# Optimization experiments

Hardware: AMD Instinct MI355X
Metric: run time of the kernel (lower is better)

Reference implementation:

```python
import jax, jax.numpy as jnp
import numpy as np

NUM_HEADS = 12
NUM_LANDMARKS = 64
PINV_ITERS = 6


def moore_penrose_iter_pinv(x, iters=PINV_ITERS):
    # x: [..., m, m]
    abs_x = jnp.abs(x)
    col = abs_x.sum(axis=-1)
    row = abs_x.sum(axis=-2)
    z = jnp.swapaxes(x, -1, -2) / (jnp.max(col) * jnp.max(row))
    I = jnp.eye(x.shape[-1], dtype=x.dtype)
    for _ in range(iters):
        xz = x @ z
        z = 0.25 * z @ (13.0 * I - xz @ (15.0 * I - xz @ (7.0 * I - xz)))
    return z


def setup_inputs() -> dict:
    key = jax.random.key(0)
    k1, k2, k3, k4 = jax.random.split(key, 4)
    B, N, C = 2, 2048, 768
    x = jax.random.normal(k1, (B, N, C), dtype=jnp.float32)
    w_qkv = jax.random.normal(k2, (3 * C, C), dtype=jnp.float32) * 0.02
    w_proj = jax.random.normal(k3, (C, C), dtype=jnp.float32) * 0.02
    b_proj = jax.random.normal(k4, (C,), dtype=jnp.float32) * 0.02
    return {"x": x, "w_qkv": w_qkv, "w_proj": w_proj, "b_proj": b_proj}


def reference(x, w_qkv, w_proj, b_proj):
    B, N, C = x.shape
    H = NUM_HEADS
    m = NUM_LANDMARKS
    d = C // H
    scale = d ** -0.5
    original_N = N

    rem = N % m
    if rem > 0:  # pad at the FRONT of the sequence, as in the torch code
        x = jnp.pad(x, ((0, 0), (m - rem, 0), (0, 0)))
        N = x.shape[1]

    qkv = x @ w_qkv.T  # [B, N, 3C]
    q, k, v = jnp.split(qkv, 3, axis=-1)
    # [B, N, C] -> [B, H, N, d]
    to_heads = lambda t: t.reshape(B, N, H, d).transpose(0, 2, 1, 3)
    q, k, v = to_heads(q), to_heads(k), to_heads(v)
    q = q * scale

    l = N // m  # segment length per landmark (N is a multiple of m after padding)
    # '(n l) d -> n d' mean over l: landmarks [B, H, m, d]
    q_landmarks = q.reshape(B, H, m, l, d).mean(axis=3)
    k_landmarks = k.reshape(B, H, m, l, d).mean(axis=3)

    sim1 = jnp.einsum('bhnd,bhmd->bhnm', q, k_landmarks)          # [B,H,N,m]
    sim2 = jnp.einsum('bhid,bhjd->bhij', q_landmarks, k_landmarks)  # [B,H,m,m]
    sim3 = jnp.einsum('bhmd,bhnd->bhmn', q_landmarks, k)          # [B,H,m,N]

    attn1 = jax.nn.softmax(sim1, axis=-1)
    attn2 = jax.nn.softmax(sim2, axis=-1)
    attn3 = jax.nn.softmax(sim3, axis=-1)

    attn2_inv = moore_penrose_iter_pinv(attn2, PINV_ITERS)

    attn = (attn1 @ attn2_inv) @ attn3            # [B,H,N,N] full attention map
    out = attn1 @ (attn2_inv @ (attn3 @ v))       # [B,H,N,d]

    out = out.transpose(0, 2, 1, 3).reshape(B, N, C)
    out = out[:, -original_N:]
    out = out @ w_proj.T + b_proj
    return out, attn
```

## Files before the change

kernel.cpp:

```cpp
#include <hip/hip_runtime.h>
#include <math.h>

#define BQ 2
#define NQ 2048
#define CQ 768
#define HQ 12
#define DQ 64
#define MQ 64
#define LQ 32
#define C3 2304
#define BH 24
#define BN 4096

typedef short bf16x8 __attribute__((ext_vector_type(8)));
typedef float f32x4 __attribute__((ext_vector_type(4)));

__device__ inline void atomicMaxPosF(float* addr, float v) {
  atomicMax((int*)addr, __float_as_int(v));
}

__device__ inline void f2pair(float f, ushort& hi, ushort& lo) {
  union { float f; unsigned u; } a; a.f = f;
  hi = (ushort)(a.u >> 16);
  union { unsigned u; float f; } h; h.u = ((unsigned)hi) << 16;
  union { float f; unsigned u; } b; b.f = f - h.f;
  lo = (ushort)(b.u >> 16);
}

__device__ inline void stage_plane(const ushort* __restrict__ g, int ld,
                                   ushort* l, int t) {
#pragma unroll
  for (int i = 0; i < 4; ++i) {
    int flat = t + i * 256;
    int row = flat >> 3;
    int ch = (flat & 7) ^ (row & 7);
    __builtin_amdgcn_global_load_lds(
        (const __attribute__((address_space(1))) void*)(g + (size_t)row * ld + ch * 8),
        (__attribute__((address_space(3))) void*)(l + flat * 8), 16, 0, 0);
  }
}

__device__ inline bf16x8 rdfrag(const ushort* p, int row, int kb) {
  return *(const bf16x8*)((const char*)p + row * 128 + (kb ^ ((row & 7) << 4)));
}

__global__ __launch_bounds__(256) void gemm_bt3(
    const ushort* __restrict__ Ah, const ushort* __restrict__ Al,
    const ushort* __restrict__ Bh, const ushort* __restrict__ Bl,
    const float* __restrict__ bias, float* __restrict__ C,
    int Kdim, int lda, int ldb, int ldc, int qscale, int zH,
    long long sAb, long long sAh, long long sBb, long long sBh,
    long long sCb, long long sCh)
{
  __shared__ __align__(16) ushort lds[32768];
  ushort* LAh = lds;
  ushort* LAl = lds + 8192;
  ushort* LBh = lds + 16384;
  ushort* LBl = lds + 24576;
  const int t = threadIdx.x;
  const int z = blockIdx.z;
  const int b = z / zH, h = z % zH;
  const size_t aoff = (size_t)b * sAb + (size_t)h * sAh + (size_t)blockIdx.x * 128 * lda;
  const size_t boff = (size_t)b * sBb + (size_t)h * sBh + (size_t)blockIdx.y * 128 * ldb;
  const ushort* pAh = Ah + aoff;
  const ushort* pAl = Al + aoff;
  const ushort* pBh = Bh + boff;
  const ushort* pBl = Bl + boff;
  float* Cp = C + (size_t)b * sCb + (size_t)h * sCh;
  const int lane = t & 63, wv = t >> 6, wm = wv >> 1, wn = wv & 1;
  f32x4 zz = {0.f, 0.f, 0.f, 0.f};
  f32x4 acc[4][4] = {{zz, zz, zz, zz}, {zz, zz, zz, zz},
                     {zz, zz, zz, zz}, {zz, zz, zz, zz}};
  for (int k0 = 0; k0 < Kdim; k0 += 64) {
    stage_plane(pAh + k0, lda, LAh, t);
    stage_plane(pAl + k0, lda, LAl, t);
    stage_plane(pBh + k0, ldb, LBh, t);
    stage_plane(pBl + k0, ldb, LBl, t);
    __syncthreads();
#pragma unroll
    for (int kh = 0; kh < 2; ++kh) {
      const int kb = kh * 64 + ((lane >> 4) * 16);
      bf16x8 aH[4], aL[4], bHf[4], bLf[4];
#pragma unroll
      for (int i = 0; i < 4; ++i) {
        int ra = wm * 64 + i * 16 + (lane & 15);
        int rb = wn * 64 + i * 16 + (lane & 15);
        aH[i] = rdfrag(LAh, ra, kb);
        aL[i] = rdfrag(LAl, ra, kb);
        bHf[i] = rdfrag(LBh, rb, kb);
        bLf[i] = rdfrag(LBl, rb, kb);
      }
#pragma unroll
      for (int i = 0; i < 4; ++i)
#pragma unroll
        for (int j = 0; j < 4; ++j) {
          acc[i][j] = __builtin_amdgcn_mfma_f32_16x16x32_bf16(aH[i], bHf[j], acc[i][j], 0, 0, 0);
          acc[i][j] = __builtin_amdgcn_mfma_f32_16x16x32_bf16(aH[i], bLf[j], acc[i][j], 0, 0, 0);
          acc[i][j] = __builtin_amdgcn_mfma_f32_16x16x32_bf16(aL[i], bHf[j], acc[i][j], 0, 0, 0);
        }
    }
    __syncthreads();
  }
#pragma unroll
  for (int i = 0; i < 4; ++i)
#pragma unroll
    for (int j = 0; j < 4; ++j) {
      int row = blockIdx.x * 128 + wm * 64 + i * 16 + (lane >> 4) * 4;
      int col = blockIdx.y * 128 + wn * 64 + j * 16 + (lane & 15);
      float badd = bias ? bias[col] : 0.0f;
      float sc = (qscale && col < CQ) ? 0.125f : 1.0f;
#pragma unroll
      for (int r = 0; r < 4; ++r)
        Cp[(size_t)(row + r) * ldc + col] = acc[i][j][r] * sc + badd;
    }
}

__global__ void convert_planes(const float* __restrict__ src, ushort* __restrict__ hi,
                               ushort* __restrict__ lo, int n4)
{
  int i = blockIdx.x * 256 + threadIdx.x;
  if (i >= n4) return;
  float4 v = ((const float4*)src)[i];
  ushort4 H, L;
  f2pair(v.x, H.x, L.x); f2pair(v.y, H.y, L.y);
  f2pair(v.z, H.z, L.z); f2pair(v.w, H.w, L.w);
  ((ushort4*)hi)[i] = H;
  ((ushort4*)lo)[i] = L;
}

__device__ inline int swzb(int row, int kbyte) {
  return row * 128 + (kbyte ^ ((row & 7) << 4));
}

__device__ inline bf16x8 ldfrag(const ushort* plane, int row, int kbyte) {
  return *(const bf16x8*)((const char*)plane + swzb(row, kbyte));
}

__device__ inline void stage_nt(const float* __restrict__ src, int ld,
                                ushort* ph, ushort* pl, int t) {
#pragma unroll
  for (int rep = 0; rep < 4; ++rep) {
    int idx = t + rep * 256;
    int row = idx >> 4, f4 = idx & 15;
    float4 v = *(const float4*)(src + (size_t)row * ld + f4 * 4);
    ushort h0, h1, h2, h3, l0, l1, l2, l3;
    f2pair(v.x, h0, l0); f2pair(v.y, h1, l1);
    f2pair(v.z, h2, l2); f2pair(v.w, h3, l3);
    int byt = row * 128 + ((f4 * 8) ^ ((row & 7) << 4));
    *(ushort4*)((char*)ph + byt) = make_ushort4(h0, h1, h2, h3);
    *(ushort4*)((char*)pl + byt) = make_ushort4(l0, l1, l2, l3);
  }
}

__device__ inline void stage_nn(const float* __restrict__ src, int ld,
                                ushort* ph, ushort* pl, int t) {
#pragma unroll
  for (int rep = 0; rep < 4; ++rep) {
    int idx = t + rep * 256;
    int krow = idx >> 4, f4 = idx & 15;
    float4 v = *(const float4*)(src + (size_t)krow * ld + f4 * 4);
    float vv[4] = {v.x, v.y, v.z, v.w};
#pragma unroll
    for (int c = 0; c < 4; ++c) {
      int n = f4 * 4 + c;
      ushort hi, lo;
      f2pair(vv[c], hi, lo);
      int byt = n * 128 + ((krow * 2) ^ ((n & 7) << 4));
      *(ushort*)((char*)ph + byt) = hi;
      *(ushort*)((char*)pl + byt) = lo;
    }
  }
}

__device__ inline void tile_mma(const ushort* Ah, const ushort* Al,
                                const ushort* Bh, const ushort* Bl,
                                f32x4 acc[2][2], int lane, int wm, int wn) {
  bf16x8 aH[2][2], aL[2][2], bH[2][2], bL[2][2];
#pragma unroll
  for (int mi = 0; mi < 2; ++mi)
#pragma unroll
    for (int ki = 0; ki < 2; ++ki) {
      int kb = ki * 64 + ((lane >> 4) * 16);
      int ra = wm * 32 + mi * 16 + (lane & 15);
      int rb = wn * 32 + mi * 16 + (lane & 15);
      aH[mi][ki] = ldfrag(Ah, ra, kb);
      aL[mi][ki] = ldfrag(Al, ra, kb);
      bH[mi][ki] = ldfrag(Bh, rb, kb);
      bL[mi][ki] = ldfrag(Bl, rb, kb);
    }
#pragma unroll
  for (int mi = 0; mi < 2; ++mi)
#pragma unroll
    for (int ni = 0; ni < 2; ++ni)
#pragma unroll
      for (int ki = 0; ki < 2; ++ki) {
        acc[mi][ni] = __builtin_amdgcn_mfma_f32_16x16x32_bf16(
            aH[mi][ki], bH[ni][ki], acc[mi][ni], 0, 0, 0);
        acc[mi][ni] = __builtin_amdgcn_mfma_f32_16x16x32_bf16(
            aH[mi][ki], bL[ni][ki], acc[mi][ni], 0, 0, 0);
        acc[mi][ni] = __builtin_amdgcn_mfma_f32_16x16x32_bf16(
            aL[mi][ki], bH[ni][ki], acc[mi][ni], 0, 0, 0);
      }
}

__global__ __launch_bounds__(256) void gemm_heads_mfma(
    const float* __restrict__ A, const float* __restrict__ Bsrc,
    float* __restrict__ Cm,
    int kTilesPerSplit, int transB, int nBH,
    long long sAb, long long sAh, int lda,
    long long sBb, long long sBh, int ldb,
    long long sCb, long long sCh, int ldc, long long sCsplit,
    ushort* __restrict__ Hout, ushort* __restrict__ Lout)
{
  __shared__ __align__(16) ushort lds[16384];
  ushort* Ah = lds; ushort* Al = lds + 4096;
  ushort* Bh = lds + 8192; ushort* Bl = lds + 12288;
  const int t = threadIdx.x;
  const int z = blockIdx.z;
  const int split = z / nBH;
  const int bh = z % nBH;
  const int b = bh / HQ, h = bh % HQ;
  const float* Ap = A + (size_t)b * sAb + (size_t)h * sAh;
  const float* Bp = Bsrc + (size_t)b * sBb + (size_t)h * sBh;
  const int m0 = blockIdx.x * 64, n0 = blockIdx.y * 64;
  const int lane = t & 63, wv = t >> 6, wm = wv >> 1, wn = wv & 1;
  f32x4 zz = {0.f, 0.f, 0.f, 0.f};
  f32x4 acc[2][2] = {{zz, zz}, {zz, zz}};
  const int kbase = split * kTilesPerSplit * 64;
  for (int kt = 0; kt < kTilesPerSplit; ++kt) {
    int k0 = kbase + kt * 64;
    stage_nt(Ap + (size_t)m0 * lda + k0, lda, Ah, Al, t);
    if (transB)
      stage_nt(Bp + (size_t)n0 * ldb + k0, ldb, Bh, Bl, t);
    else
      stage_nn(Bp + (size_t)k0 * ldb + n0, ldb, Bh, Bl, t);
    __syncthreads();
    tile_mma(Ah, Al, Bh, Bl, acc, lane, wm, wn);
    __syncthreads();
  }
  if (Hout) {
    ushort* Hp = Hout + (size_t)b * sCb + (size_t)h * sCh + (size_t)split * sCsplit;
    ushort* Lp = Lout + (size_t)b * sCb + (size_t)h * sCh + (size_t)split * sCsplit;
#pragma unroll
    for (int mi = 0; mi < 2; ++mi)
#pragma unroll
      for (int ni = 0; ni < 2; ++ni) {
        int row = m0 + wm * 32 + mi * 16 + (lane >> 4) * 4;
        int col = n0 + wn * 32 + ni * 16 + (lane & 15);
#pragma unroll
        for (int r = 0; r < 4; ++r) {
          ushort hi, lo;
          f2pair(acc[mi][ni][r], hi, lo);
          Hp[(size_t)(row + r) * ldc + col] = hi;
          Lp[(size_t)(row + r) * ldc + col] = lo;
        }
      }
  } else {
    float* Cp = Cm + (size_t)b * sCb + (size_t)h * sCh + (size_t)split * sCsplit;
#pragma unroll
    for (int mi = 0; mi < 2; ++mi)
#pragma unroll
      for (int ni = 0; ni < 2; ++ni) {
        int row = m0 + wm * 32 + mi * 16 + (lane >> 4) * 4;
        int col = n0 + wn * 32 + ni * 16 + (lane & 15);
#pragma unroll
        for (int r = 0; r < 4; ++r)
          Cp[(size_t)(row + r) * ldc + col] = acc[mi][ni][r];
      }
  }
}

__global__ void landmarks_kernel(const float* __restrict__ qkv,
                                 float* __restrict__ ql, float* __restrict__ kl)
{
  int idx = blockIdx.x * 256 + threadIdx.x;
  int sel = idx / 98304;
  int r = idx % 98304;
  int bh = r / 4096;
  int b = bh / HQ, h = bh % HQ;
  int i = (r % 4096) / 64;
  int dd = r & 63;
  const float* base = qkv + (size_t)(b * NQ + i * LQ) * C3 + sel * CQ + h * 64 + dd;
  float s = 0.f;
#pragma unroll
  for (int j = 0; j < LQ; ++j) s += base[(size_t)j * C3];
  float* outp = sel ? kl : ql;
  outp[bh * 4096 + i * 64 + dd] = s * (1.0f / 32.0f);
}

__global__ __launch_bounds__(256) void attn2_prep(
    const float* __restrict__ ql, const float* __restrict__ kl,
    float* __restrict__ attn2, float* __restrict__ scal)
{
  __shared__ float Q[64][68], Kl[64][68], S[64][68];
  __shared__ float red[128];
  const int bh = blockIdx.x;
  const int t = threadIdx.x;
#pragma unroll
  for (int rep = 0; rep < 4; ++rep) {
    int idx = t + rep * 256;
    int row = idx >> 4, f4 = idx & 15;
    *(float4*)&Q[row][f4 * 4] = *(const float4*)(ql + (size_t)bh * 4096 + row * 64 + f4 * 4);
    *(float4*)&Kl[row][f4 * 4] = *(const float4*)(kl + (size_t)bh * 4096 + row * 64 + f4 * 4);
  }
  __syncthreads();
  {
    int i = t >> 2;
    int jb = (t & 3) * 16;
    for (int jj = 0; jj < 16; ++jj) {
      int j = jb + jj;
      float s2 = 0.f;
#pragma unroll
      for (int kk = 0; kk < 64; ++kk) s2 = fmaf(Q[i][kk], Kl[j][kk], s2);
      S[i][j] = s2;
    }
  }
  __syncthreads();
  if (t < 64) {
    float mx = -INFINITY;
    for (int j = 0; j < 64; ++j) mx = fmaxf(mx, S[t][j]);
    float sum = 0.f;
    for (int j = 0; j < 64; ++j) { float e = expf(S[t][j] - mx); S[t][j] = e; sum += e; }
    float inv = 1.0f / sum;
    float rs = 0.f;
    for (int j = 0; j < 64; ++j) { float v = S[t][j] * inv; S[t][j] = v; rs += v; }
    red[t] = rs;
  }
  __syncthreads();
  if (t < 64) {
    float cs = 0.f;
    for (int i = 0; i < 64; ++i) cs += S[i][t];
    red[64 + t] = cs;
  }
  __syncthreads();
  if (t == 0) {
    float m1 = red[0], m2 = red[64];
    for (int j = 1; j < 64; ++j) { m1 = fmaxf(m1, red[j]); m2 = fmaxf(m2, red[64 + j]); }
    atomicMaxPosF(scal + 0, m1);
    atomicMaxPosF(scal + 1, m2);
  }
  for (int idx = t; idx < 4096; idx += 256)
    attn2[(size_t)bh * 4096 + idx] = S[idx >> 6][idx & 63];
}

__device__ inline void mm64x(float (*D)[68], const float (*A)[68], const float (*B)[68],
                             int t, float scale)
{
  const int lane = t & 63, wv = t >> 6;
  float bcol[64];
#pragma unroll
  for (int kk = 0; kk < 64; ++kk) bcol[kk] = B[kk][lane];
#pragma unroll
  for (int rr = 0; rr < 4; ++rr) {
    int i = wv * 4 + rr;
    float acc2 = 0.f;
#pragma unroll
    for (int kk = 0; kk < 64; ++kk) acc2 = fmaf(A[i][kk], bcol[kk], acc2);
    D[i][lane] = acc2 * scale;
  }
}

__global__ __launch_bounds__(1024) void pinv_kernel(
    const float* __restrict__ attn2, const float* __restrict__ scal,
    float* __restrict__ zinv)
{
  __shared__ float X[64][68], Z[64][68], P[64][68], Q[64][68], R[64][68];
  const int bh = blockIdx.x;
  const int t = threadIdx.x;
  const float denom = scal[0] * scal[1];
#pragma unroll
  for (int rep = 0; rep < 4; ++rep) {
    int idx = t + rep * 1024;
    X[idx >> 6][idx & 63] = attn2[(size_t)bh * 4096 + idx];
  }
  __syncthreads();
#pragma unroll
  for (int rep = 0; rep < 4; ++rep) {
    int idx = t + rep * 1024;
    int i = idx >> 6, j = idx & 63;
    Z[j][i] = X[i][j] / denom;
  }
  for (int it = 0; it < 6; ++it) {
    __syncthreads();
    mm64x(P, X, Z, t, 1.0f);
    __syncthreads();
    for (int idx = t; idx < 4096; idx += 1024) {
      int i = idx >> 6, j = idx & 63;
      Q[i][j] = (i == j ? 7.0f : 0.0f) - P[i][j];
    }
    __syncthreads();
    mm64x(R, P, Q, t, 1.0f);
    __syncthreads();
    for (int idx = t; idx < 4096; idx += 1024) {
      int i = idx >> 6, j = idx & 63;
      Q[i][j] = (i == j ? 15.0f : 0.0f) - R[i][j];
    }
    __syncthreads();
    mm64x(R, P, Q, t, 1.0f);
    __syncthreads();
    for (int idx = t; idx < 4096; idx += 1024) {
      int i = idx >> 6, j = idx & 63;
      Q[i][j] = (i == j ? 13.0f : 0.0f) - R[i][j];
    }
    __syncthreads();
    mm64x(P, Z, Q, t, 0.25f);
    __syncthreads();
    for (int idx = t; idx < 4096; idx += 1024) {
      int i = idx >> 6, j = idx & 63;
      Z[i][j] = P[i][j];
    }
  }
  __syncthreads();
  for (int idx = t; idx < 4096; idx += 1024)
    zinv[(size_t)bh * 4096 + idx] = Z[idx >> 6][idx & 63];
}

__global__ __launch_bounds__(256) void attn1_kernel(
    const float* __restrict__ qkv, const float* __restrict__ kl,
    ushort* __restrict__ A1h, ushort* __restrict__ A1l)
{
  __shared__ float qs[64][68], klt[64][68];
  const int n0 = blockIdx.x * 64;
  const int bh = blockIdx.y;
  const int b = bh / HQ, h = bh % HQ;
  const int t = threadIdx.x;
#pragma unroll
  for (int rep = 0; rep < 4; ++rep) {
    int idx = t + rep * 256;
    int row = idx >> 4, f4 = idx & 15;
    *(float4*)&qs[row][f4 * 4] =
        *(const float4*)(qkv + (size_t)(b * NQ + n0 + row) * C3 + h * 64 + f4 * 4);
    float4 kv = *(const float4*)(kl + (size_t)bh * 4096 + row * 64 + f4 * 4);
    klt[f4 * 4 + 0][row] = kv.x; klt[f4 * 4 + 1][row] = kv.y;
    klt[f4 * 4 + 2][row] = kv.z; klt[f4 * 4 + 3][row] = kv.w;
  }
  __syncthreads();
  const int lane = t & 63, wv = t >> 6;
  float bcol[64];
#pragma unroll
  for (int kk = 0; kk < 64; ++kk) bcol[kk] = klt[kk][lane];
  for (int rr = 0; rr < 16; ++rr) {
    int i = wv * 16 + rr;
    float s = 0.f;
#pragma unroll
    for (int kk = 0; kk < 64; ++kk) s = fmaf(qs[i][kk], bcol[kk], s);
    float mx = s;
#pragma unroll
    for (int off = 32; off; off >>= 1) mx = fmaxf(mx, __shfl_xor(mx, off));
    float e = expf(s - mx);
    float sum = e;
#pragma unroll
    for (int off = 32; off; off >>= 1) sum += __shfl_xor(sum, off);
    float v = e / sum;
    ushort hi, lo;
    f2pair(v, hi, lo);
    size_t o = ((size_t)(b * NQ + n0 + i)) * CQ + h * 64 + lane;
    A1h[o] = hi;
    A1l[o] = lo;
  }
}

__global__ __launch_bounds__(256) void sim3_fused(
    const float* __restrict__ ql, const float* __restrict__ qkv,
    ushort* __restrict__ eth, ushort* __restrict__ etl,
    float* __restrict__ rspart, float* __restrict__ evp)
{
  __shared__ __align__(16) ushort lds[32768];
  __shared__ float rsq[2][64];
  const int chunk = blockIdx.x, bh = blockIdx.y;
  const int b = bh / HQ, h = bh % HQ;
  const int n0 = chunk * 64;
  const int t = threadIdx.x;
  const int lane = t & 63, wv = t >> 6, wm = wv >> 1, wn = wv & 1;
  ushort* Aqh = lds;         ushort* Aql = lds + 4096;
  ushort* Bkh = lds + 8192;  ushort* Bkl = lds + 12288;
  ushort* EH  = lds + 16384; ushort* EL  = lds + 20480;
  ushort* ETH = lds + 24576; ushort* ETL = lds + 28672;
  ushort* vTh = lds;         ushort* vTl = lds + 4096;

  stage_nt(ql + (size_t)bh * 4096, 64, Aqh, Aql, t);
  stage_nt(qkv + (size_t)(b * NQ + n0) * C3 + CQ + h * 64, C3, Bkh, Bkl, t);
  __syncthreads();
  f32x4 zz = {0.f, 0.f, 0.f, 0.f};
  f32x4 acc[2][2] = {{zz, zz}, {zz, zz}};
  tile_mma(Aqh, Aql, Bkh, Bkl, acc, lane, wm, wn);
  float e[2][2][4];
#pragma unroll
  for (int mi = 0; mi < 2; ++mi)
#pragma unroll
    for (int ni = 0; ni < 2; ++ni)
#pragma unroll
      for (int r = 0; r < 4; ++r) {
        float ev = __expf(acc[mi][ni][r]);
        e[mi][ni][r] = ev;
        int m = wm * 32 + mi * 16 + ((lane >> 4) << 2) + r;
        int n = wn * 32 + ni * 16 + (lane & 15);
        ushort hi, lo;
        f2pair(ev, hi, lo);
        *(ushort*)((char*)EH + swzb(m, n * 2)) = hi;
        *(ushort*)((char*)EL + swzb(m, n * 2)) = lo;
        *(ushort*)((char*)ETH + swzb(n, m * 2)) = hi;
        *(ushort*)((char*)ETL + swzb(n, m * 2)) = lo;
      }
#pragma unroll
  for (int mi = 0; mi < 2; ++mi)
#pragma unroll
    for (int r = 0; r < 4; ++r) {
      float s = e[mi][0][r] + e[mi][1][r];
      s += __shfl_xor(s, 1); s += __shfl_xor(s, 2);
      s += __shfl_xor(s, 4); s += __shfl_xor(s, 8);
      if ((lane & 15) == 0)
        rsq[wn][wm * 32 + mi * 16 + ((lane >> 4) << 2) + r] = s;
    }
  __syncthreads();
  stage_nn(qkv + (size_t)(b * NQ + n0) * C3 + 2 * CQ + h * 64, C3, vTh, vTl, t);
  if (t < 64)
    rspart[(size_t)(bh * 32 + chunk) * 64 + t] = rsq[0][t] + rsq[1][t];
  {
    ushort* gh = eth + (size_t)(bh * 32 + chunk) * 4096;
    ushort* gl = etl + (size_t)(bh * 32 + chunk) * 4096;
#pragma unroll
    for (int r2 = 0; r2 < 2; ++r2) {
      int c8 = t + r2 * 256;
      *(bf16x8*)(gh + c8 * 8) = *(const bf16x8*)(ETH + c8 * 8);
      *(bf16x8*)(gl + c8 * 8) = *(const bf16x8*)(ETL + c8 * 8);
    }
  }
  __syncthreads();
  f32x4 acc2[2][2] = {{zz, zz}, {zz, zz}};
  tile_mma(EH, EL, vTh, vTl, acc2, lane, wm, wn);
  float* evpp = evp + (size_t)(bh * 32 + chunk) * 4096;
#pragma unroll
  for (int mi = 0; mi < 2; ++mi)
#pragma unroll
    for (int ni = 0; ni < 2; ++ni) {
      int m = wm * 32 + mi * 16 + ((lane >> 4) << 2);
      int d = wn * 32 + ni * 16 + (lane & 15);
#pragma unroll
      for (int r = 0; r < 4; ++r)
        evpp[(m + r) * 64 + d] = acc2[mi][ni][r];
    }
}

__global__ __launch_bounds__(256) void pinv_apply(
    const float* __restrict__ rspart, const float* __restrict__ evp,
    const float* __restrict__ zinv, float* __restrict__ uu,
    ushort* __restrict__ zph, ushort* __restrict__ zpl)
{
  __shared__ __align__(16) ushort lds[16384];
  __shared__ float rs[64];
  ushort* EvTh = lds;        ushort* EvTl = lds + 4096;
  ushort* ZAh  = lds + 8192; ushort* ZAl  = lds + 12288;
  const int bh = blockIdx.x;
  const int t = threadIdx.x;
  const int lane = t & 63, wv = t >> 6, wm = wv >> 1, wn = wv & 1;
  if (t < 64) {
    float s = 0.f;
#pragma unroll
    for (int c = 0; c < 32; ++c) s += rspart[(size_t)(bh * 32 + c) * 64 + t];
    rs[t] = s;
  }
#pragma unroll
  for (int rep = 0; rep < 16; ++rep) {
    int idx = t + rep * 256;
    int m = idx >> 6, d = idx & 63;
    float s = 0.f;
    for (int c = 0; c < 32; ++c) s += evp[(size_t)(bh * 32 + c) * 4096 + idx];
    ushort hi, lo;
    f2pair(s, hi, lo);
    *(ushort*)((char*)EvTh + swzb(d, m * 2)) = hi;
    *(ushort*)((char*)EvTl + swzb(d, m * 2)) = lo;
  }
  __syncthreads();
#pragma unroll
  for (int rep = 0; rep < 16; ++rep) {
    int idx = t + rep * 256;
    int i = idx >> 6, m = idx & 63;
    float v = zinv[(size_t)bh * 4096 + idx] / rs[m];
    ushort hi, lo;
    f2pair(v, hi, lo);
    *(ushort*)((char*)ZAh + swzb(i, m * 2)) = hi;
    *(ushort*)((char*)ZAl + swzb(i, m * 2)) = lo;
  }
  __syncthreads();
  f32x4 zz = {0.f, 0.f, 0.f, 0.f};
  f32x4 acc[2][2] = {{zz, zz}, {zz, zz}};
  tile_mma(ZAh, ZAl, EvTh, EvTl, acc, lane, wm, wn);
#pragma unroll
  for (int mi = 0; mi < 2; ++mi)
#pragma unroll
    for (int ni = 0; ni < 2; ++ni) {
      int i = wm * 32 + mi * 16 + ((lane >> 4) << 2);
      int d = wn * 32 + ni * 16 + (lane & 15);
#pragma unroll
      for (int r = 0; r < 4; ++r)
        uu[(size_t)bh * 4096 + (i + r) * 64 + d] = acc[mi][ni][r];
    }
#pragma unroll
  for (int r2 = 0; r2 < 2; ++r2) {
    int c8 = t + r2 * 256;
    *(bf16x8*)(zph + (size_t)bh * 4096 + c8 * 8) = *(const bf16x8*)(ZAh + c8 * 8);
    *(bf16x8*)(zpl + (size_t)bh * 4096 + c8 * 8) = *(const bf16x8*)(ZAl + c8 * 8);
  }
}

__global__ __launch_bounds__(256) void t_chunk_kernel(
    const ushort* __restrict__ zph, const ushort* __restrict__ zpl,
    const ushort* __restrict__ eth, const ushort* __restrict__ etl,
    ushort* __restrict__ tth, ushort* __restrict__ ttl)
{
  __shared__ __align__(16) ushort lds[16384];
  __shared__ float Tt[64][65];
  ushort* ZAh = lds;        ushort* ZAl = lds + 4096;
  ushort* EBh = lds + 8192; ushort* EBl = lds + 12288;
  const int chunk = blockIdx.x, bh = blockIdx.y;
  const int t = threadIdx.x;
  const int lane = t & 63, wv = t >> 6, wm = wv >> 1, wn = wv & 1;
  const ushort* geh = eth + (size_t)(bh * 32 + chunk) * 4096;
  const ushort* gel = etl + (size_t)(bh * 32 + chunk) * 4096;
#pragma unroll
  for (int r2 = 0; r2 < 2; ++r2) {
    int c8 = t + r2 * 256;
    *(bf16x8*)(ZAh + c8 * 8) = *(const bf16x8*)(zph + (size_t)bh * 4096 + c8 * 8);
    *(bf16x8*)(ZAl + c8 * 8) = *(const bf16x8*)(zpl + (size_t)bh * 4096 + c8 * 8);
    *(bf16x8*)(EBh + c8 * 8) = *(const bf16x8*)(geh + c8 * 8);
    *(bf16x8*)(EBl + c8 * 8) = *(const bf16x8*)(gel + c8 * 8);
  }
  __syncthreads();
  f32x4 zz = {0.f, 0.f, 0.f, 0.f};
  f32x4 acc[2][2] = {{zz, zz}, {zz, zz}};
  tile_mma(ZAh, ZAl, EBh, EBl, acc, lane, wm, wn);
#pragma unroll
  for (int mi = 0; mi < 2; ++mi)
#pragma unroll
    for (int ni = 0; ni < 2; ++ni) {
      int i = wm * 32 + mi * 16 + ((lane >> 4) << 2);
      int n = wn * 32 + ni * 16 + (lane & 15);
#pragma unroll
      for (int r = 0; r < 4; ++r)
        Tt[i + r][n] = acc[mi][ni][r];
    }
  __syncthreads();
  const size_t base = ((size_t)bh * 2048 + chunk * 64) * 64;
#pragma unroll
  for (int rep = 0; rep < 16; ++rep) {
    int idx = t + rep * 256;
    int n = idx >> 6, i = idx & 63;
    ushort hi, lo;
    f2pair(Tt[i][n], hi, lo);
    tth[base + n * 64 + i] = hi;
    ttl[base + n * 64 + i] = lo;
  }
}

__global__ void init_scal(float* s)
{
  if (threadIdx.x < 2) s[threadIdx.x] = 0.0f;
}

extern "C" void kernel_launch(void* const* d_in, const int* in_sizes, int n_in,
                              void* d_out, int out_size, void* d_ws, size_t ws_size,
                              hipStream_t stream)
{
  const float* x = (const float*)d_in[0];
  const float* w_qkv = (const float*)d_in[1];
  const float* w_proj = (const float*)d_in[2];
  const float* b_proj = (const float*)d_in[3];
  float* out = (float*)d_out;
  float* R = out + (size_t)BQ * NQ * CQ;

  float* QKV = R;
  float* EVP = R + 9437184;
  float* UU  = R + 12582912;
  float* RSP = R + 12681216;
  ushort* et_h = (ushort*)(R + 12730368);
  ushort* et_l = et_h + 3145728;
  ushort* zp_h = et_l + 3145728;
  ushort* zp_l = zp_h + 98304;
  ushort* xp_h = zp_l + 98304;
  ushort* xp_l = xp_h + 3145728;
  ushort* wq_h = xp_l + 3145728;
  ushort* wq_l = wq_h + 1769472;
  ushort* gt_h = wq_l + 1769472;
  ushort* gt_l = gt_h + 1179648;

  float* ws = (float*)d_ws;
  float* QL = ws;
  float* KL = QL + 98304;
  float* A2 = KL + 98304;
  float* ZI = A2 + 98304;
  float* SC = ZI + 98304;
  ushort* a1_h = (ushort*)(SC + 32);
  ushort* a1_l = a1_h + 3145728;
  ushort* tt_h = a1_l + 3145728;
  ushort* tt_l = tt_h + 3145728;

  init_scal<<<1, 64, 0, stream>>>(SC);

  convert_planes<<<3072, 256, 0, stream>>>(x, xp_h, xp_l, 786432);
  convert_planes<<<1728, 256, 0, stream>>>(w_qkv, wq_h, wq_l, 442368);

  gemm_bt3<<<dim3(32, 18, 1), 256, 0, stream>>>(
      xp_h, xp_l, wq_h, wq_l, nullptr, QKV,
      CQ, CQ, CQ, C3, 1, 1, 0, 0, 0, 0, 0, 0);

  landmarks_kernel<<<768, 256, 0, stream>>>(QKV, QL, KL);
  attn2_prep<<<24, 256, 0, stream>>>(QL, KL, A2, SC);
  pinv_kernel<<<24, 1024, 0, stream>>>(A2, SC, ZI);
  attn1_kernel<<<dim3(32, 24), 256, 0, stream>>>(QKV, KL, a1_h, a1_l);

  sim3_fused<<<dim3(32, 24), 256, 0, stream>>>(QL, QKV, et_h, et_l, RSP, EVP);
  pinv_apply<<<24, 256, 0, stream>>>(RSP, EVP, ZI, UU, zp_h, zp_l);
  gemm_heads_mfma<<<dim3(12, 1, 24), 256, 0, stream>>>(
      w_proj, UU, nullptr, 1, 1, 24,
      0, 64, CQ,
      (long long)HQ * 4096, 4096, 64,
      (long long)CQ * CQ, 64, CQ, 0, gt_h, gt_l);
  t_chunk_kernel<<<dim3(32, 24), 256, 0, stream>>>(zp_h, zp_l, et_h, et_l, tt_h, tt_l);

  gemm_bt3<<<dim3(16, 6, 2), 256, 0, stream>>>(
      a1_h, a1_l, gt_h, gt_l, b_proj, out,
      CQ, CQ, CQ, CQ, 0, 1,
      (long long)NQ * CQ, 0, (long long)CQ * CQ, 0, (long long)NQ * CQ, 0);

  gemm_bt3<<<dim3(16, 16, 24), 256, 0, stream>>>(
      a1_h, a1_l, tt_h, tt_l, nullptr, R,
      64, CQ, 64, 2048, 0, HQ,
      (long long)NQ * CQ, 64,
      (long long)HQ * 131072, 131072,
      (long long)HQ * 4194304LL, 4194304);
}
```

Measured before the change: 465.0 us.

## Parallelize partial reductions, fuse pinv identity subtraction, fold scalar init

```diff
diff --git a/kernel.cpp b/kernel.cpp
--- a/kernel.cpp
+++ b/kernel.cpp
@@ -116,9 +116,10 @@
 }
 
 __global__ void convert_planes(const float* __restrict__ src, ushort* __restrict__ hi,
-                               ushort* __restrict__ lo, int n4)
+                               ushort* __restrict__ lo, int n4, float* __restrict__ sc)
 {
   int i = blockIdx.x * 256 + threadIdx.x;
+  if (sc && blockIdx.x == 0 && threadIdx.x < 2) sc[threadIdx.x] = 0.0f;
   if (i >= n4) return;
   float4 v = ((const float4*)src)[i];
   ushort4 H, L;
@@ -360,11 +361,28 @@
   }
 }
 
+__device__ inline void mm64d(float (*D)[68], const float (*A)[68], const float (*B)[68],
+                             int t, float c, float scale)
+{
+  const int lane = t & 63, wv = t >> 6;
+  float bcol[64];
+#pragma unroll
+  for (int kk = 0; kk < 64; ++kk) bcol[kk] = ((kk == lane) ? c : 0.0f) - B[kk][lane];
+#pragma unroll
+  for (int rr = 0; rr < 4; ++rr) {
+    int i = wv * 4 + rr;
+    float acc2 = 0.f;
+#pragma unroll
+    for (int kk = 0; kk < 64; ++kk) acc2 = fmaf(A[i][kk], bcol[kk], acc2);
+    D[i][lane] = acc2 * scale;
+  }
+}
+
 __global__ __launch_bounds__(1024) void pinv_kernel(
     const float* __restrict__ attn2, const float* __restrict__ scal,
     float* __restrict__ zinv)
 {
-  __shared__ float X[64][68], Z[64][68], P[64][68], Q[64][68], R[64][68];
+  __shared__ float X[64][68], B0[64][68], B1[64][68], B2[64][68], B3[64][68];
   const int bh = blockIdx.x;
   const int t = threadIdx.x;
   const float denom = scal[0] * scal[1];
@@ -378,41 +396,31 @@
   for (int rep = 0; rep < 4; ++rep) {
     int idx = t + rep * 1024;
     int i = idx >> 6, j = idx & 63;
-    Z[j][i] = X[i][j] / denom;
-  }
+    B0[j][i] = X[i][j] / denom;
+  }
+  float (*pZ)[68] = B0;
+  float (*pP)[68] = B1;
+  float (*pQ)[68] = B2;
+  float (*pR)[68] = B3;
   for (int it = 0; it < 6; ++it) {
     __syncthreads();
-    mm64x(P, X, Z, t, 1.0f);
+    mm64x(pP, X, pZ, t, 1.0f);
     __syncthreads();
-    for (int idx = t; idx < 4096; idx += 1024) {
-      int i = idx >> 6, j = idx & 63;
-      Q[i][j] = (i == j ? 7.0f : 0.0f) - P[i][j];
-    }
+    mm64d(pQ, pP, pP, t, 7.0f, 1.0f);
     __syncthreads();
-    mm64x(R, P, Q, t, 1.0f);
+    mm64d(pR, pP, pQ, t, 15.0f, 1.0f);
     __syncthreads();
-    for (int idx = t; idx < 4096; idx += 1024) {
-      int i = idx >> 6, j = idx & 63;
-      Q[i][j] = (i == j ? 15.0f : 0.0f) - R[i][j];
-    }
-    __syncthreads();
-    mm64x(R, P, Q, t, 1.0f);
-    __syncthreads();
-    for (int idx = t; idx < 4096; idx += 1024) {
-      int i = idx >> 6, j = idx & 63;
-      Q[i][j] = (i == j ? 13.0f : 0.0f) - R[i][j];
-    }
-    __syncthreads();
-    mm64x(P, Z, Q, t, 0.25f);
-    __syncthreads();
-    for (int idx = t; idx < 4096; idx += 1024) {
-      int i = idx >> 6, j = idx & 63;
-      Z[i][j] = P[i][j];
-    }
-  }
-  __syncthreads();
-  for (int idx = t; idx < 4096; idx += 1024)
-    zinv[(size_t)bh * 4096 + idx] = Z[idx >> 6][idx & 63];
+    mm64d(pQ, pZ, pR, t, 13.0f, 0.25f);
+    float (*tmp)[68] = pZ;
+    pZ = pQ;
+    pQ = tmp;
+  }
+  __syncthreads();
+#pragma unroll
+  for (int rep = 0; rep < 4; ++rep) {
+    int idx = t + rep * 1024;
+    zinv[(size_t)bh * 4096 + idx] = pZ[idx >> 6][idx & 63];
+  }
 }
 
 __global__ __launch_bounds__(256) void attn1_kernel(
@@ -542,8 +550,29 @@
     }
 }
 
+__global__ void rs_final(const float* __restrict__ rspart, float* __restrict__ rsf)
+{
+  int g = blockIdx.x * 256 + threadIdx.x;
+  if (g >= 1536) return;
+  int bh = g >> 6, j = g & 63;
+  float s = 0.f;
+#pragma unroll
+  for (int c = 0; c < 32; ++c) s += rspart[(size_t)(bh * 32 + c) * 64 + j];
+  rsf[g] = s;
+}
+
+__global__ void reduce_ev(const float* __restrict__ evp, float* __restrict__ ev)
+{
+  int g = blockIdx.x * 256 + threadIdx.x;
+  int bh = g >> 12, idx2 = g & 4095;
+  float s = 0.f;
+#pragma unroll
+  for (int c = 0; c < 32; ++c) s += evp[(size_t)(bh * 32 + c) * 4096 + idx2];
+  ev[g] = s;
+}
+
 __global__ __launch_bounds__(256) void pinv_apply(
-    const float* __restrict__ rspart, const float* __restrict__ evp,
+    const float* __restrict__ rsf, const float* __restrict__ ev,
     const float* __restrict__ zinv, float* __restrict__ uu,
     ushort* __restrict__ zph, ushort* __restrict__ zpl)
 {
@@ -554,23 +583,8 @@
   const int bh = blockIdx.x;
   const int t = threadIdx.x;
   const int lane = t & 63, wv = t >> 6, wm = wv >> 1, wn = wv & 1;
-  if (t < 64) {
-    float s = 0.f;
-#pragma unroll
-    for (int c = 0; c < 32; ++c) s += rspart[(size_t)(bh * 32 + c) * 64 + t];
-    rs[t] = s;
-  }
-#pragma unroll
-  for (int rep = 0; rep < 16; ++rep) {
-    int idx = t + rep * 256;
-    int m = idx >> 6, d = idx & 63;
-    float s = 0.f;
-    for (int c = 0; c < 32; ++c) s += evp[(size_t)(bh * 32 + c) * 4096 + idx];
-    ushort hi, lo;
-    f2pair(s, hi, lo);
-    *(ushort*)((char*)EvTh + swzb(d, m * 2)) = hi;
-    *(ushort*)((char*)EvTl + swzb(d, m * 2)) = lo;
-  }
+  if (t < 64) rs[t] = rsf[bh * 64 + t];
+  stage_nn(ev + (size_t)bh * 4096, 64, EvTh, EvTl, t);
   __syncthreads();
 #pragma unroll
   for (int rep = 0; rep < 16; ++rep) {
@@ -653,11 +667,6 @@
   }
 }
 
-__global__ void init_scal(float* s)
-{
-  if (threadIdx.x < 2) s[threadIdx.x] = 0.0f;
-}
-
 extern "C" void kernel_launch(void* const* d_in, const int* in_sizes, int n_in,
                               void* d_out, int out_size, void* d_ws, size_t ws_size,
                               hipStream_t stream)
@@ -671,9 +680,11 @@
 
   float* QKV = R;
   float* EVP = R + 9437184;
-  float* UU  = R + 12582912;
-  float* RSP = R + 12681216;
-  ushort* et_h = (ushort*)(R + 12730368);
+  float* EV  = R + 12582912;
+  float* UU  = R + 12681216;
+  float* RSP = R + 12779520;
+  float* RSF = R + 12828672;
+  ushort* et_h = (ushort*)(R + 12830208);
   ushort* et_l = et_h + 3145728;
   ushort* zp_h = et_l + 3145728;
   ushort* zp_l = zp_h + 98304;
@@ -695,10 +706,8 @@
   ushort* tt_h = a1_l + 3145728;
   ushort* tt_l = tt_h + 3145728;
 
-  init_scal<<<1, 64, 0, stream>>>(SC);
-
-  convert_planes<<<3072, 256, 0, stream>>>(x, xp_h, xp_l, 786432);
-  convert_planes<<<1728, 256, 0, stream>>>(w_qkv, wq_h, wq_l, 442368);
+  convert_planes<<<3072, 256, 0, stream>>>(x, xp_h, xp_l, 786432, SC);
+  convert_planes<<<1728, 256, 0, stream>>>(w_qkv, wq_h, wq_l, 442368, nullptr);
 
   gemm_bt3<<<dim3(32, 18, 1), 256, 0, stream>>>(
       xp_h, xp_l, wq_h, wq_l, nullptr, QKV,
@@ -710,7 +719,9 @@
   attn1_kernel<<<dim3(32, 24), 256, 0, stream>>>(QKV, KL, a1_h, a1_l);
 
   sim3_fused<<<dim3(32, 24), 256, 0, stream>>>(QL, QKV, et_h, et_l, RSP, EVP);
-  pinv_apply<<<24, 256, 0, stream>>>(RSP, EVP, ZI, UU, zp_h, zp_l);
+  rs_final<<<6, 256, 0, stream>>>(RSP, RSF);
+  reduce_ev<<<384, 256, 0, stream>>>(EVP, EV);
+  pinv_apply<<<24, 256, 0, stream>>>(RSF, EV, ZI, UU, zp_h, zp_l);
   gemm_heads_mfma<<<dim3(12, 1, 24), 256, 0, stream>>>(
       w_proj, UU, nullptr, 1, 1, 24,
       0, 64, CQ,
```

After: 465.5 us. No clear change (+0.1%).
